# Kernel optimization log

Hardware: AMD Instinct MI355X
Metric: run time of the kernel (lower is better)

The kernel has to match this reference:

```python
import jax, jax.numpy as jnp
import numpy as np

# Constants from the original module
C_BASE = 1e-14
N_BITS = 4
C_RATIO = 100 * (2 ** N_BITS - 1)  # 1500
INIT_C1_SCALED = 0.924458
N_ITER = 2 * 9  # 18 sequential charge-integration steps per patch


def setup_inputs() -> dict:
    key = jax.random.key(0)
    k1, k2 = jax.random.split(key)
    x = jax.random.normal(k1, (4608, 4608), dtype=jnp.float32)
    weight = jax.random.normal(k2, (3, 3), dtype=jnp.float32)
    return {"x": x, "weight": weight}


def reference(x, weight):
    """3x3 stride-3 'conv' realized as a per-patch switched-capacitor
    charge-integration recurrence (2-phase clock, 18 Euler steps), vectorized
    over all patches with a single lax.scan over the 18 steps.

    Per-patch recurrence (matching the repo's two-phase switched-cap Euler step):
      phase PHI1 (even i): sampling cap C_s(i) charges to vin(i): q_samp = C_s(i)*vin(i)
      phase PHI2 (odd  i): sampled charge transfers onto integrating cap: q_int += q_samp
    Readout: voltage = q_int / c2 * C_RATIO ; output = -voltage.
    """
    W, H = x.shape
    nw, nh = W // 3, H // 3
    # Non-overlapping 3x3 patches -> (nw, nh, 9), matching x_slice.flatten()
    patches = x[: nw * 3, : nh * 3].reshape(nw, 3, nh, 3)
    patches = patches.transpose(0, 2, 1, 3).reshape(nw, nh, 9)

    # padded_weight: (9,4) with flattened weight in bit-column 0, then repeat x2 -> (18,4)
    wflat = weight.reshape(9)
    padded = jnp.zeros((9, 4), dtype=x.dtype).at[:, 0].set(wflat)
    bits_arr = jnp.repeat(padded, 2, axis=0)  # (18, 4)
    bit_weights = (2.0 ** jnp.arange(4)).astype(x.dtype)
    cs = C_BASE * (bits_arr @ bit_weights)  # (18,) sampling capacitance per step

    vin = jnp.repeat(patches, 2, axis=-1)  # (nw, nh, 18) input voltage per step

    c1 = INIT_C1_SCALED * C_BASE
    c2 = c1 * C_RATIO  # integrating capacitance

    def step(state, i):
        q_int, q_samp = state  # each (nw, nh)
        p1 = jnp.asarray(i % 2 == 0, x.dtype)  # PHI1 clock
        p2 = 1.0 - p1                          # PHI2 clock
        q_samp_new = p1 * cs[i] * vin[..., i]
        q_int_new = q_int + p2 * q_samp
        return (q_int_new, q_samp_new), None

    init = (jnp.zeros((nw, nh), x.dtype), jnp.zeros((nw, nh), x.dtype))
    (q_int, _), _ = jax.lax.scan(step, init, jnp.arange(N_ITER))

    voltage = q_int / c2 * C_RATIO  # readout of charge_trace[-1, 0]
    return (-voltage).reshape(-1)
```

## Files before the change

### kernel.cpp

```cpp
#include <hip/hip_runtime.h>


__global__ __launch_bounds__(256) void conv3x3_s3_kernel(
    const float* __restrict__ x,
    const float* __restrict__ w,
    float* __restrict__ out)
{
    constexpr int W   = 4608;
    constexpr int NH  = 1536;
    constexpr int JQ  = NH / 4;

    const int tid = blockIdx.x * blockDim.x + threadIdx.x;
    const int i   = tid / JQ;
    const int jq  = tid - i * JQ;

    const float w00 = w[0], w01 = w[1], w02 = w[2];
    const float w10 = w[3], w11 = w[4], w12 = w[5];
    const float w20 = w[6], w21 = w[7], w22 = w[8];

    const float* base = x + (size_t)(3 * i) * W + 12 * jq;

    float acc0 = 0.f, acc1 = 0.f, acc2 = 0.f, acc3 = 0.f;

    #pragma unroll
    for (int a = 0; a < 3; ++a) {
        const float4* p = reinterpret_cast<const float4*>(base + (size_t)a * W);
        const float4 v0 = p[0];
        const float4 v1 = p[1];
        const float4 v2 = p[2];

        float wa0, wa1, wa2;
        if (a == 0)      { wa0 = w00; wa1 = w01; wa2 = w02; }
        else if (a == 1) { wa0 = w10; wa1 = w11; wa2 = w12; }
        else             { wa0 = w20; wa1 = w21; wa2 = w22; }

        acc0 += wa0 * v0.x + wa1 * v0.y + wa2 * v0.z;
        acc1 += wa0 * v0.w + wa1 * v1.x + wa2 * v1.y;
        acc2 += wa0 * v1.z + wa1 * v1.w + wa2 * v2.x;
        acc3 += wa0 * v2.y + wa1 * v2.z + wa2 * v2.w;
    }

    const float scale = -1.0f / 0.924458f;

    float4 r;
    r.x = acc0 * scale;
    r.y = acc1 * scale;
    r.z = acc2 * scale;
    r.w = acc3 * scale;

    float4* o = reinterpret_cast<float4*>(out + (size_t)i * NH + 4 * jq);
    *o = r;
}

extern "C" void kernel_launch(void* const* d_in, const int* in_sizes, int n_in,
                              void* d_out, int out_size, void* d_ws, size_t ws_size,
                              hipStream_t stream)
{
    const float* x = (const float*)d_in[0];
    const float* w = (const float*)d_in[1];
    float* out = (float*)d_out;

    constexpr int NW = 1536, JQ = 1536 / 4;
    const int total   = NW * JQ;
    const int block   = 256;
    const int grid    = total / block;

    conv3x3_s3_kernel<<<grid, block, 0, stream>>>(x, w, out);
}
```

Before: 19.08 us.

## Stage input tiles through LDS with fully coalesced float4 loads

Each block loads a contiguous 12x768 input tile into shared memory using coalesced float4 loads, then computes 4x256 outputs from LDS. This replaces the strided per-thread global loads, which touched scattered cache lines. It costs 36 KB of LDS per block, which may lower occupancy, plus a barrier and possible bank conflicts on the strided LDS reads.

```diff
diff --git a/kernel.cpp b/kernel.cpp
--- a/kernel.cpp
+++ b/kernel.cpp
@@ -1,33 +1,67 @@
 #include <hip/hip_runtime.h>
 
 
-__global__ __launch_bounds__(256) void conv3x3_s3_kernel(
+constexpr int W        = 4608;
+constexpr int NH       = 1536;
+constexpr int TILE_OR  = 4;
+constexpr int TILE_OC  = 256;
+constexpr int IN_ROWS  = 3 * TILE_OR;
+constexpr int IN_COLS  = 3 * TILE_OC;
+constexpr int F4_ROW   = IN_COLS / 4;
+constexpr int TOTAL_F4 = IN_ROWS * F4_ROW;
+constexpr int BLOCK    = 256;
+constexpr int F4_PER_T = TOTAL_F4 / BLOCK;
+
+__global__ __launch_bounds__(BLOCK) void conv3x3_s3_lds(
     const float* __restrict__ x,
     const float* __restrict__ w,
     float* __restrict__ out)
 {
-    constexpr int W   = 4608;
-    constexpr int NH  = 1536;
-    constexpr int JQ  = NH / 4;
+    __shared__ float4 lds[TOTAL_F4];
 
-    const int tid = blockIdx.x * blockDim.x + threadIdx.x;
-    const int i   = tid / JQ;
-    const int jq  = tid - i * JQ;
+    const int t    = threadIdx.x;
+    const int tile = blockIdx.x;
+    constexpr int TILES_PER_ROW = NH / TILE_OC;
+    const int ti = tile / TILES_PER_ROW;
+    const int tj = tile - ti * TILES_PER_ROW;
+
+    const int R0 = ti * IN_ROWS;
+    const int C0 = tj * IN_COLS;
+
+    const float* xb = x + (size_t)R0 * W + C0;
+
+    float4 tmp[F4_PER_T];
+    #pragma unroll
+    for (int k = 0; k < F4_PER_T; ++k) {
+        const int f = t + k * BLOCK;
+        const int r = f / F4_ROW;
+        const int c = f - r * F4_ROW;
+        tmp[k] = *reinterpret_cast<const float4*>(xb + (size_t)r * W + 4 * c);
+    }
 
     const float w00 = w[0], w01 = w[1], w02 = w[2];
     const float w10 = w[3], w11 = w[4], w12 = w[5];
     const float w20 = w[6], w21 = w[7], w22 = w[8];
 
-    const float* base = x + (size_t)(3 * i) * W + 12 * jq;
+    #pragma unroll
+    for (int k = 0; k < F4_PER_T; ++k)
+        lds[t + k * BLOCK] = tmp[k];
+
+    __syncthreads();
+
+    const int wv = t >> 6;
+    const int l  = t & 63;
+
+    const float* lf = reinterpret_cast<const float*>(lds);
 
     float acc0 = 0.f, acc1 = 0.f, acc2 = 0.f, acc3 = 0.f;
 
     #pragma unroll
     for (int a = 0; a < 3; ++a) {
-        const float4* p = reinterpret_cast<const float4*>(base + (size_t)a * W);
-        const float4 v0 = p[0];
-        const float4 v1 = p[1];
-        const float4 v2 = p[2];
+        const float* row = lf + (size_t)(3 * wv + a) * IN_COLS + 12 * l;
+        const float4 v0 = *reinterpret_cast<const float4*>(row);
+        const float4 v1 = *reinterpret_cast<const float4*>(row + 4);
+        const float4 v2 = *reinterpret_cast<const float4*>(row + 8);
 
         float wa0, wa1, wa2;
         if (a == 0)      { wa0 = w00; wa1 = w01; wa2 = w02; }
@@ -41,15 +75,14 @@
     }
 
     const float scale = -1.0f / 0.924458f;
+    float4 r4;
+    r4.x = acc0 * scale;
+    r4.y = acc1 * scale;
+    r4.z = acc2 * scale;
+    r4.w = acc3 * scale;
 
-    float4 r;
-    r.x = acc0 * scale;
-    r.y = acc1 * scale;
-    r.z = acc2 * scale;
-    r.w = acc3 * scale;
-
-    float4* o = reinterpret_cast<float4*>(out + (size_t)i * NH + 4 * jq);
-    *o = r;
+    float* o = out + (size_t)(TILE_OR * ti + wv) * NH + TILE_OC * tj + 4 * l;
+    *reinterpret_cast<float4*>(o) = r4;
 }
 
 extern "C" void kernel_launch(void* const* d_in, const int* in_sizes, int n_in,
@@ -60,10 +93,6 @@
     const float* w = (const float*)d_in[1];
     float* out = (float*)d_out;
 
-    constexpr int NW = 1536, JQ = 1536 / 4;
-    const int total   = NW * JQ;
-    const int block   = 256;
-    const int grid    = total / block;
-
-    conv3x3_s3_kernel<<<grid, block, 0, stream>>>(x, w, out);
+    constexpr int GRID = (NH / TILE_OR) * (NH / TILE_OC);
+    conv3x3_s3_lds<<<GRID, BLOCK, 0, stream>>>(x, w, out);
 }
```

Measured after the change: 19.60 us. 1.03x slower.

## Use persistent grid-stride kernel with 768-thread blocks and batched loads

Applied to the files above, without the earlier changes.

Replaces the one-quad-per-thread launch of 2304 blocks with a persistent launch of 256 blocks of 768 threads. Each thread walks 3 tasks in a grid-stride loop, and each task issues all nine float4 loads before doing the arithmetic. The aim is to cut block scheduling overhead and raise memory-level parallelism on a purely bandwidth-bound kernel. The cost is fewer waves in flight overall, higher register pressure from the unrolled loop, and stride patterns that may coalesce less well.

```diff
diff --git a/kernel.cpp b/kernel.cpp
--- a/kernel.cpp
+++ b/kernel.cpp
@@ -1,55 +1,72 @@
 #include <hip/hip_runtime.h>
 
 
-__global__ __launch_bounds__(256) void conv3x3_s3_kernel(
+constexpr int W      = 4608;
+constexpr int NH     = 1536;
+constexpr int QPR    = NH / 4;
+constexpr int NQUADS = NH * QPR;
+constexpr int BLOCK  = 768;
+constexpr int GRID   = 256;
+constexpr int STRIDE = BLOCK * GRID;
+constexpr int TASKS  = NQUADS / STRIDE;
+
+__global__ __launch_bounds__(BLOCK) void conv3x3_s3_persist(
     const float* __restrict__ x,
     const float* __restrict__ w,
     float* __restrict__ out)
 {
-    constexpr int W   = 4608;
-    constexpr int NH  = 1536;
-    constexpr int JQ  = NH / 4;
-
-    const int tid = blockIdx.x * blockDim.x + threadIdx.x;
-    const int i   = tid / JQ;
-    const int jq  = tid - i * JQ;
+    const int t0 = blockIdx.x * BLOCK + threadIdx.x;
 
     const float w00 = w[0], w01 = w[1], w02 = w[2];
     const float w10 = w[3], w11 = w[4], w12 = w[5];
     const float w20 = w[6], w21 = w[7], w22 = w[8];
 
-    const float* base = x + (size_t)(3 * i) * W + 12 * jq;
-
-    float acc0 = 0.f, acc1 = 0.f, acc2 = 0.f, acc3 = 0.f;
+    const float scale = -1.0f / 0.924458f;
 
     #pragma unroll
-    for (int a = 0; a < 3; ++a) {
-        const float4* p = reinterpret_cast<const float4*>(base + (size_t)a * W);
-        const float4 v0 = p[0];
-        const float4 v1 = p[1];
-        const float4 v2 = p[2];
+    for (int k = 0; k < TASKS; ++k) {
+        const unsigned tau = (unsigned)(t0 + k * STRIDE);
+        const unsigned row = tau / QPR;
+        const unsigned q   = tau - row * QPR;
 
-        float wa0, wa1, wa2;
-        if (a == 0)      { wa0 = w00; wa1 = w01; wa2 = w02; }
-        else if (a == 1) { wa0 = w10; wa1 = w11; wa2 = w12; }
-        else             { wa0 = w20; wa1 = w21; wa2 = w22; }
+        const float* base = x + (size_t)(3 * row) * W + 12 * q;
 
-        acc0 += wa0 * v0.x + wa1 * v0.y + wa2 * v0.z;
-        acc1 += wa0 * v0.w + wa1 * v1.x + wa2 * v1.y;
-        acc2 += wa0 * v1.z + wa1 * v1.w + wa2 * v2.x;
-        acc3 += wa0 * v2.y + wa1 * v2.z + wa2 * v2.w;
+        float4 v[9];
+        #pragma unroll
+        for (int a = 0; a < 3; ++a) {
+            const float4* p = reinterpret_cast<const float4*>(base + (size_t)a * W);
+            v[3 * a + 0] = p[0];
+            v[3 * a + 1] = p[1];
+            v[3 * a + 2] = p[2];
+        }
+
+        float acc0 = 0.f, acc1 = 0.f, acc2 = 0.f, acc3 = 0.f;
+        #pragma unroll
+        for (int a = 0; a < 3; ++a) {
+            float wa0, wa1, wa2;
+            if (a == 0)      { wa0 = w00; wa1 = w01; wa2 = w02; }
+            else if (a == 1) { wa0 = w10; wa1 = w11; wa2 = w12; }
+            else             { wa0 = w20; wa1 = w21; wa2 = w22; }
+
+            const float4 v0 = v[3 * a + 0];
+            const float4 v1 = v[3 * a + 1];
+            const float4 v2 = v[3 * a + 2];
+
+            acc0 += wa0 * v0.x + wa1 * v0.y + wa2 * v0.z;
+            acc1 += wa0 * v0.w + wa1 * v1.x + wa2 * v1.y;
+            acc2 += wa0 * v1.z + wa1 * v1.w + wa2 * v2.x;
+            acc3 += wa0 * v2.y + wa1 * v2.z + wa2 * v2.w;
+        }
+
+        float4 r4;
+        r4.x = acc0 * scale;
+        r4.y = acc1 * scale;
+        r4.z = acc2 * scale;
+        r4.w = acc3 * scale;
+
+        float* o = out + (size_t)row * NH + 4 * q;
+        *reinterpret_cast<float4*>(o) = r4;
     }
-
-    const float scale = -1.0f / 0.924458f;
-
-    float4 r;
-    r.x = acc0 * scale;
-    r.y = acc1 * scale;
-    r.z = acc2 * scale;
-    r.w = acc3 * scale;
-
-    float4* o = reinterpret_cast<float4*>(out + (size_t)i * NH + 4 * jq);
-    *o = r;
 }
 
 extern "C" void kernel_launch(void* const* d_in, const int* in_sizes, int n_in,
@@ -60,10 +77,5 @@
     const float* w = (const float*)d_in[1];
     float* out = (float*)d_out;
 
-    constexpr int NW = 1536, JQ = 1536 / 4;
-    const int total   = NW * JQ;
-    const int block   = 256;
-    const int grid    = total / block;
-
-    conv3x3_s3_kernel<<<grid, block, 0, stream>>>(x, w, out);
+    conv3x3_s3_persist<<<GRID, BLOCK, 0, stream>>>(x, w, out);
 }
```

Result: slower. 19.83 us (+3.9%).
